# Kernel tuning notes

Hardware: AMD Instinct MI355X
Metric: run time of the kernel (lower is better)

The kernel has to match this reference:

```python
import jax, jax.numpy as jnp
import numpy as np

B, S, D, R = 32, 2048, 1280, 50  # batch, max seq len, embed dim, reduce_size


def setup_inputs() -> dict:
    key = jax.random.key(0)
    kx, kl = jax.random.split(key)
    x = jax.random.normal(kx, (B, S, D), dtype=jnp.float32)
    # contiguous prefix masks with variable lengths in [S//2, S]
    lengths = jax.random.randint(kl, (B,), S // 2, S + 1)
    mask = (jnp.arange(S)[None, :] < lengths[:, None]).astype(jnp.int32)
    return {"x": x, "mask": mask, "getstd": 1}


def _window_onehot(mask):
    """Build [B, S, R] float assignment matrix mapping each valid position to its window.

    Per sample (length L): m = L // R windows; gap = L - m*R leftover positions.
    gapleft = ceil(gap/2) leading windows of size m+1, mid = R-gap windows of size m,
    gapright = gap//2 trailing windows of size m+1 (matches torch loop exactly).
    """
    seqs = jnp.sum(mask, axis=1)          # [B]
    L = seqs[:, None]                     # [B, 1]
    m = L // R                            # min_window_size, >=1 for our lengths
    gap = L - m * R
    gl = gap // 2 + (gap % 2)             # gapleft (gets the extra one if gap odd)
    mid = R - gap
    msafe = jnp.maximum(m, 1)             # guard division
    pos = jnp.arange(S)[None, :]          # [1, S]
    firstend = gl * (m + 1)
    midend = firstend + mid * m
    seg = jnp.where(
        pos < firstend,
        pos // (m + 1),
        jnp.where(
            pos < midend,
            gl + (pos - firstend) // msafe,
            gl + mid + (pos - midend) // (m + 1),
        ),
    )                                      # [B, S]
    valid = pos < L                        # [B, S]
    onehot = (seg[:, :, None] == jnp.arange(R)[None, None, :]) & valid[:, :, None]
    return onehot.astype(jnp.float32)      # [B, S, R]


def reference(x, mask, getstd):
    onehot = _window_onehot(mask)                         # [B, S, R]
    counts = jnp.sum(onehot, axis=1)                      # [B, R]
    sums = jnp.einsum('bsr,bsd->brd', onehot, x)          # window sums
    mean = sums / counts[:, :, None]                      # [B, R, D]
    if getstd:
        xm = jnp.einsum('bsr,brd->bsd', onehot, mean)     # per-position window mean
        diffsq = (x - xm) ** 2
        var = jnp.einsum('bsr,bsd->brd', onehot, diffsq) / counts[:, :, None]
        return mean, jnp.sqrt(var)
    return mean
```

## Files before the change

kernel.cpp:

```cpp
#include <hip/hip_runtime.h>

#define B 32
#define S 2048
#define D 1280
#define R 50

__global__ __launch_bounds__(256) void compute_len_kernel(
    const int* __restrict__ mask, int* __restrict__ Lbuf)
{
    const int b = blockIdx.x;
    const int t = threadIdx.x;
    const int* __restrict__ mrow = mask + (size_t)b * S;

    int sum = 0;
    for (int i = t; i < S; i += 256) sum += mrow[i];

    for (int off = 32; off > 0; off >>= 1) sum += __shfl_down(sum, off, 64);

    __shared__ int ws[4];
    const int wave = t >> 6;
    const int lane = t & 63;
    if (lane == 0) ws[wave] = sum;
    __syncthreads();
    if (t == 0) Lbuf[b] = ws[0] + ws[1] + ws[2] + ws[3];
}

__global__ __launch_bounds__(320) void window_stats_kernel(
    const float* __restrict__ x, const int* __restrict__ Lbuf,
    float* __restrict__ out, int getstd)
{
    const int blk = blockIdx.x;
    const int b = blk / R;
    const int r = blk - b * R;

    const int L   = Lbuf[b];
    const int m   = L / R;
    const int gap = L - m * R;
    const int gl  = (gap + 1) >> 1;
    const int mid = R - gap;

    int start, cnt;
    if (r < gl) {
        start = r * (m + 1);
        cnt   = m + 1;
    } else if (r < gl + mid) {
        start = gl * (m + 1) + (r - gl) * m;
        cnt   = m;
    } else {
        start = gl * (m + 1) + mid * m + (r - (gl + mid)) * (m + 1);
        cnt   = m + 1;
    }

    const int t = threadIdx.x;
    const float4* __restrict__ xr =
        reinterpret_cast<const float4*>(x + ((size_t)b * S + (size_t)start) * D) + t;

    float s0 = 0.f, s1 = 0.f, s2 = 0.f, s3 = 0.f;
    float q0 = 0.f, q1 = 0.f, q2 = 0.f, q3 = 0.f;

    for (int i = 0; i < cnt; ++i) {
        float4 v = xr[(size_t)i * (D / 4)];
        s0 += v.x; q0 = fmaf(v.x, v.x, q0);
        s1 += v.y; q1 = fmaf(v.y, v.y, q1);
        s2 += v.z; q2 = fmaf(v.z, v.z, q2);
        s3 += v.w; q3 = fmaf(v.w, v.w, q3);
    }

    const float inv = 1.0f / (float)cnt;
    const float m0 = s0 * inv, m1 = s1 * inv, m2 = s2 * inv, m3 = s3 * inv;

    const size_t obase = ((size_t)b * R + r) * D;
    float4 mv; mv.x = m0; mv.y = m1; mv.z = m2; mv.w = m3;
    reinterpret_cast<float4*>(out + obase)[t] = mv;

    if (getstd) {
        float v0 = fmaxf(fmaf(-m0, m0, q0 * inv), 0.f);
        float v1 = fmaxf(fmaf(-m1, m1, q1 * inv), 0.f);
        float v2 = fmaxf(fmaf(-m2, m2, q2 * inv), 0.f);
        float v3 = fmaxf(fmaf(-m3, m3, q3 * inv), 0.f);
        float4 sv;
        sv.x = sqrtf(v0); sv.y = sqrtf(v1); sv.z = sqrtf(v2); sv.w = sqrtf(v3);
        reinterpret_cast<float4*>(out + (size_t)B * R * D + obase)[t] = sv;
    }
}

extern "C" void kernel_launch(void* const* d_in, const int* in_sizes, int n_in,
                              void* d_out, int out_size, void* d_ws, size_t ws_size,
                              hipStream_t stream)
{
    const float* x    = (const float*)d_in[0];
    const int*   mask = (const int*)d_in[1];
    float*       out  = (float*)d_out;
    int*         Lbuf = (int*)d_ws;

    const int getstd = (out_size >= 2 * B * R * D) ? 1 : 0;

    compute_len_kernel<<<B, 256, 0, stream>>>(mask, Lbuf);
    window_stats_kernel<<<B * R, 320, 0, stream>>>(x, Lbuf, out, getstd);
}
```

Baseline: 57.75 us.

## Fuse mask-length reduction into window stats kernel and unroll row loop

Removes the separate length-reduction kernel: each block now reads its sample's mask row with int4 loads and reduces it in-block before computing window bounds. This drops one launch and the dependency between kernels, but has all 50 blocks per sample redundantly read the 8KB mask row. The accumulation loop is also unrolled by four with two independent accumulator sets to keep more loads in flight.

Measured after the change: 50.33 us. 12.8% less time.

```diff
diff --git a/kernel.cpp b/kernel.cpp
--- a/kernel.cpp
+++ b/kernel.cpp
@@ -5,35 +5,32 @@
 #define D 1280
 #define R 50
 
-__global__ __launch_bounds__(256) void compute_len_kernel(
-    const int* __restrict__ mask, int* __restrict__ Lbuf)
-{
-    const int b = blockIdx.x;
-    const int t = threadIdx.x;
-    const int* __restrict__ mrow = mask + (size_t)b * S;
-
-    int sum = 0;
-    for (int i = t; i < S; i += 256) sum += mrow[i];
-
-    for (int off = 32; off > 0; off >>= 1) sum += __shfl_down(sum, off, 64);
-
-    __shared__ int ws[4];
-    const int wave = t >> 6;
-    const int lane = t & 63;
-    if (lane == 0) ws[wave] = sum;
-    __syncthreads();
-    if (t == 0) Lbuf[b] = ws[0] + ws[1] + ws[2] + ws[3];
-}
-
-__global__ __launch_bounds__(320) void window_stats_kernel(
-    const float* __restrict__ x, const int* __restrict__ Lbuf,
+__global__ __launch_bounds__(320) void window_stats_fused(
+    const float* __restrict__ x, const int* __restrict__ mask,
     float* __restrict__ out, int getstd)
 {
     const int blk = blockIdx.x;
     const int b = blk / R;
     const int r = blk - b * R;
+    const int t = threadIdx.x;
 
-    const int L   = Lbuf[b];
+    const int4* __restrict__ mrow = reinterpret_cast<const int4*>(mask + (size_t)b * S);
+    int lsum;
+    {
+        int4 v0 = mrow[t];
+        lsum = v0.x + v0.y + v0.z + v0.w;
+        if (t + 320 < S / 4) {
+            int4 v1 = mrow[t + 320];
+            lsum += v1.x + v1.y + v1.z + v1.w;
+        }
+    }
+    #pragma unroll
+    for (int off = 32; off > 0; off >>= 1) lsum += __shfl_down(lsum, off, 64);
+    __shared__ int wsum[5];
+    if ((t & 63) == 0) wsum[t >> 6] = lsum;
+    __syncthreads();
+    const int L = wsum[0] + wsum[1] + wsum[2] + wsum[3] + wsum[4];
+
     const int m   = L / R;
     const int gap = L - m * R;
     const int gl  = (gap + 1) >> 1;
@@ -51,20 +48,51 @@
         cnt   = m + 1;
     }
 
-    const int t = threadIdx.x;
     const float4* __restrict__ xr =
         reinterpret_cast<const float4*>(x + ((size_t)b * S + (size_t)start) * D) + t;
 
-    float s0 = 0.f, s1 = 0.f, s2 = 0.f, s3 = 0.f;
-    float q0 = 0.f, q1 = 0.f, q2 = 0.f, q3 = 0.f;
+    float sA0 = 0.f, sA1 = 0.f, sA2 = 0.f, sA3 = 0.f;
+    float qA0 = 0.f, qA1 = 0.f, qA2 = 0.f, qA3 = 0.f;
+    float sB0 = 0.f, sB1 = 0.f, sB2 = 0.f, sB3 = 0.f;
+    float qB0 = 0.f, qB1 = 0.f, qB2 = 0.f, qB3 = 0.f;
 
-    for (int i = 0; i < cnt; ++i) {
-        float4 v = xr[(size_t)i * (D / 4)];
-        s0 += v.x; q0 = fmaf(v.x, v.x, q0);
-        s1 += v.y; q1 = fmaf(v.y, v.y, q1);
-        s2 += v.z; q2 = fmaf(v.z, v.z, q2);
-        s3 += v.w; q3 = fmaf(v.w, v.w, q3);
+    int i = 0;
+    for (; i + 4 <= cnt; i += 4) {
+        float4 a = xr[(size_t)(i + 0) * (D / 4)];
+        float4 c = xr[(size_t)(i + 1) * (D / 4)];
+        float4 d = xr[(size_t)(i + 2) * (D / 4)];
+        float4 e = xr[(size_t)(i + 3) * (D / 4)];
+
+        sA0 += a.x; qA0 = fmaf(a.x, a.x, qA0);
+        sA1 += a.y; qA1 = fmaf(a.y, a.y, qA1);
+        sA2 += a.z; qA2 = fmaf(a.z, a.z, qA2);
+        sA3 += a.w; qA3 = fmaf(a.w, a.w, qA3);
+
+        sB0 += c.x; qB0 = fmaf(c.x, c.x, qB0);
+        sB1 += c.y; qB1 = fmaf(c.y, c.y, qB1);
+        sB2 += c.z; qB2 = fmaf(c.z, c.z, qB2);
+        sB3 += c.w; qB3 = fmaf(c.w, c.w, qB3);
+
+        sA0 += d.x; qA0 = fmaf(d.x, d.x, qA0);
+        sA1 += d.y; qA1 = fmaf(d.y, d.y, qA1);
+        sA2 += d.z; qA2 = fmaf(d.z, d.z, qA2);
+        sA3 += d.w; qA3 = fmaf(d.w, d.w, qA3);
+
+        sB0 += e.x; qB0 = fmaf(e.x, e.x, qB0);
+        sB1 += e.y; qB1 = fmaf(e.y, e.y, qB1);
+        sB2 += e.z; qB2 = fmaf(e.z, e.z, qB2);
+        sB3 += e.w; qB3 = fmaf(e.w, e.w, qB3);
     }
+    for (; i < cnt; ++i) {
+        float4 a = xr[(size_t)i * (D / 4)];
+        sA0 += a.x; qA0 = fmaf(a.x, a.x, qA0);
+        sA1 += a.y; qA1 = fmaf(a.y, a.y, qA1);
+        sA2 += a.z; qA2 = fmaf(a.z, a.z, qA2);
+        sA3 += a.w; qA3 = fmaf(a.w, a.w, qA3);
+    }
+
+    const float s0 = sA0 + sB0, s1 = sA1 + sB1, s2 = sA2 + sB2, s3 = sA3 + sB3;
+    const float q0 = qA0 + qB0, q1 = qA1 + qB1, q2 = qA2 + qB2, q3 = qA3 + qB3;
 
     const float inv = 1.0f / (float)cnt;
     const float m0 = s0 * inv, m1 = s1 * inv, m2 = s2 * inv, m3 = s3 * inv;
@@ -91,10 +119,8 @@
     const float* x    = (const float*)d_in[0];
     const int*   mask = (const int*)d_in[1];
     float*       out  = (float*)d_out;
-    int*         Lbuf = (int*)d_ws;
 
     const int getstd = (out_size >= 2 * B * R * D) ? 1 : 0;
 
-    compute_len_kernel<<<B, 256, 0, stream>>>(mask, Lbuf);
-    window_stats_kernel<<<B * R, 320, 0, stream>>>(x, Lbuf, out, getstd);
+    window_stats_fused<<<B * R, 320, 0, stream>>>(x, mask, out, getstd);
 }
```
